# Kernel optimization log

Hardware: AMD Instinct MI355X
Metric: run time of the kernel (lower is better)

Reference implementation:

```python
import jax, jax.numpy as jnp
import numpy as np


def _ln(x, g, b):
    m = x.mean(-1, keepdims=True)
    v = ((x - m) ** 2).mean(-1, keepdims=True)
    return (x - m) * jax.lax.rsqrt(v + 1e-5) * g + b


def _forward(x, fx_in, pre_w1, pre_b1, pre_w2, pre_b2, placeholder,
             ln1_g, ln1_b, px_w, px_b, pfx_w, pfx_b, slice_w, slice_b, temp,
             q_w, k_w, v_w, out_w, out_b, ln2_g, ln2_b,
             mlp_w1, mlp_b1, mlp_w2, mlp_b2,
             ln3_g, ln3_b, head_w1, head_b1, head_w2, head_b2):
    # All linear weights are stored as [in, out] (pre-transposed vs torch nn.Linear).
    B, N, _ = x.shape
    L, H = temp.shape
    dh = slice_w.shape[1]
    gelu = lambda t: jax.nn.gelu(t, approximate=False)
    # preprocess MLP (n_layers=0, res=False): Linear -> GELU -> Linear
    h = jnp.concatenate([x, fx_in], axis=-1)
    h = gelu(h @ pre_w1 + pre_b1) @ pre_w2 + pre_b2
    h = h + placeholder  # learned [D] offset
    scale = 1.0 / jnp.sqrt(jnp.asarray(dh, h.dtype))
    for i in range(L):  # loop over structurally distinct layers
        y = _ln(h, ln1_g[i], ln1_b[i])
        # project to per-head features: bhnd
        fx_mid = (y @ pfx_w[i] + pfx_b[i]).reshape(B, N, H, dh).transpose(0, 2, 1, 3)
        x_mid = (y @ px_w[i] + px_b[i]).reshape(B, N, H, dh).transpose(0, 2, 1, 3)
        # soft slice assignment over G slices
        logits = jnp.einsum('bhnd,dg->bhng', x_mid, slice_w[i]) + slice_b[i]
        sw = jax.nn.softmax(logits / temp[i][None, :, None, None], axis=-1)  # bhng
        norm = sw.sum(axis=2)  # bhg
        tok = jnp.einsum('bhnd,bhng->bhgd', fx_mid, sw) / (norm + 1e-5)[..., None]
        # attention over G=slice_num tokens
        q = tok @ q_w[i]
        k = tok @ k_w[i]
        v = tok @ v_w[i]
        attn = jax.nn.softmax(jnp.einsum('bhgd,bhmd->bhgm', q, k) * scale, axis=-1)
        out_slice = jnp.einsum('bhgm,bhmd->bhgd', attn, v)
        # deslice back to points
        out_x = jnp.einsum('bhgd,bhng->bhnd', out_slice, sw)
        out_x = out_x.transpose(0, 2, 1, 3).reshape(B, N, H * dh)
        h = h + (out_x @ out_w[i] + out_b[i])
        z = _ln(h, ln2_g[i], ln2_b[i])
        h = h + (gelu(z @ mlp_w1[i] + mlp_b1[i]) @ mlp_w2[i] + mlp_b2[i])
    z = _ln(h, ln3_g, ln3_b)
    return gelu(z @ head_w1 + head_b1) @ head_w2 + head_b2


def setup_inputs() -> dict:
    key = jax.random.key(0)
    B, N, D, H, dh, G, L = 2, 16384, 256, 8, 32, 64, 5
    SP, FUN, OUT = 2, 4, 4
    ID = H * dh  # inner_dim == n_hidden
    MR = D * 1   # mlp_ratio=1
    ks = iter(jax.random.split(key, 64))
    nrm = lambda shape, s=0.02: jax.random.normal(next(ks), shape, jnp.float32) * s
    return dict(
        x=jax.random.normal(next(ks), (B, N, SP), jnp.float32),
        fx_in=jax.random.normal(next(ks), (B, N, FUN), jnp.float32),
        pre_w1=nrm((SP + FUN, 2 * D)), pre_b1=jnp.zeros((2 * D,), jnp.float32),
        pre_w2=nrm((2 * D, D)), pre_b2=jnp.zeros((D,), jnp.float32),
        placeholder=nrm((D,)),
        ln1_g=jnp.ones((L, D), jnp.float32), ln1_b=jnp.zeros((L, D), jnp.float32),
        px_w=nrm((L, D, ID)), px_b=jnp.zeros((L, ID), jnp.float32),
        pfx_w=nrm((L, D, ID)), pfx_b=jnp.zeros((L, ID), jnp.float32),
        slice_w=nrm((L, dh, G), 0.1), slice_b=jnp.zeros((L, G), jnp.float32),
        temp=0.5 * jnp.ones((L, H), jnp.float32),
        q_w=nrm((L, dh, dh), 0.1), k_w=nrm((L, dh, dh), 0.1), v_w=nrm((L, dh, dh), 0.1),
        out_w=nrm((L, ID, D)), out_b=jnp.zeros((L, D), jnp.float32),
        ln2_g=jnp.ones((L, D), jnp.float32), ln2_b=jnp.zeros((L, D), jnp.float32),
        mlp_w1=nrm((L, D, MR)), mlp_b1=jnp.zeros((L, MR), jnp.float32),
        mlp_w2=nrm((L, MR, D)), mlp_b2=jnp.zeros((L, D), jnp.float32),
        ln3_g=jnp.ones((D,), jnp.float32), ln3_b=jnp.zeros((D,), jnp.float32),
        head_w1=nrm((D, D)), head_b1=jnp.zeros((D,), jnp.float32),
        head_w2=nrm((D, OUT)), head_b2=jnp.zeros((OUT,), jnp.float32),
    )


def reference(x, fx_in, pre_w1, pre_b1, pre_w2, pre_b2, placeholder,
              ln1_g, ln1_b, px_w, px_b, pfx_w, pfx_b, slice_w, slice_b, temp,
              q_w, k_w, v_w, out_w, out_b, ln2_g, ln2_b,
              mlp_w1, mlp_b1, mlp_w2, mlp_b2,
              ln3_g, ln3_b, head_w1, head_b1, head_w2, head_b2):
    return _forward(x, fx_in, pre_w1, pre_b1, pre_w2, pre_b2, placeholder,
                    ln1_g, ln1_b, px_w, px_b, pfx_w, pfx_b, slice_w, slice_b, temp,
                    q_w, k_w, v_w, out_w, out_b, ln2_g, ln2_b,
                    mlp_w1, mlp_b1, mlp_w2, mlp_b2,
                    ln3_g, ln3_b, head_w1, head_b1, head_w2, head_b2)
```

## Files before the change

kernel.cpp:

```cpp
#include <hip/hip_runtime.h>


#define MTOK 32768
#define NB   16384

typedef unsigned short u16;
using short8 = __attribute__((ext_vector_type(8))) short;
using f4     = __attribute__((ext_vector_type(4))) float;

__device__ __forceinline__ float bfu(u16 u) {
    return __uint_as_float(((unsigned)u) << 16);
}
__device__ __forceinline__ u16 f2bf(float f) {
    unsigned u = __float_as_uint(f);
    u += 0x7FFFu + ((u >> 16) & 1u);
    return (u16)(u >> 16);
}
__device__ __forceinline__ float ldf(const void* p, int i, int isbf) {
    return isbf ? bfu(((const u16*)p)[i]) : ((const float*)p)[i];
}
__device__ __forceinline__ float4 dec4(ushort4 u) {
    return make_float4(bfu(u.x), bfu(u.y), bfu(u.z), bfu(u.w));
}
__device__ __forceinline__ float gelu_f(float x) {
    return 0.5f * x * (1.0f + erff(x * 0.7071067811865475f));
}

typedef __attribute__((address_space(1))) const unsigned int* as1p;
typedef __attribute__((address_space(3))) unsigned int* as3p;
__device__ __forceinline__ void gload_lds16(const u16* g, u16* l) {
    __builtin_amdgcn_global_load_lds((as1p)g, (as3p)l, 16, 0, 0);
}

#define F_H      ((size_t)0)
#define F_OS     ((size_t)8388608)
#define F_TOKP   ((size_t)8421376)
#define F_NORMP  ((size_t)10518528)
#define F_TOK    ((size_t)10584064)
#define F_NORM   ((size_t)10616832)
#define F_BIAS   ((size_t)10617856)
#define F_PARAMS ((size_t)10626048)
#define F_BF     ((size_t)10858884)
#define B_PB2C 0
#define B_OUTB 256
#define B_M1B  1536
#define B_M2B  2816
#define B_HB1  4096
#define B_SP   4352
#define B_END  8192
#define U_WT     ((size_t)0)
#define WT_PRE2  0
#define WT_HEAD1 131072
#define WT_SPFX  196608
#define WT_OUT   1179648
#define WT_MLP1  1507328
#define WT_MLP2  1835008
#define WT_END   2162688
#define U_Y   ((size_t)2162688)
#define U_XM  ((size_t)10551296)
#define U_FM  ((size_t)18939904)
#define U_SW  ((size_t)27328512)

#define P_X    0
#define P_FX   65536
#define P_W1   196608
#define P_B1   199680
#define P_LN1G 200192
#define P_LN1B 201472
#define P_LN2G 202752
#define P_LN2B 204032
#define P_LN3G 205312
#define P_LN3B 205568
#define P_SLW  205824
#define P_SLB  216064
#define P_TEMP 216384
#define P_QW   216448
#define P_KW   221568
#define P_VW   226688
#define P_HW2  231808
#define P_HB2  232832
#define P_END  232836

__global__ __launch_bounds__(256) void cvt_kernel(
    const void* x, const void* fx, const void* w1, const void* b1,
    const void* l1g, const void* l1b, const void* l2g, const void* l2b,
    const void* l3g, const void* l3b, const void* slw, const void* slb,
    const void* tmp, const void* qw, const void* kw, const void* vw,
    const void* hw2, const void* hb2, float* __restrict__ P)
{
    int isbf = (((const u16*)tmp)[0] != 0);
    int idx = blockIdx.x * 256 + threadIdx.x;
    const void* s; int o;
    if      (idx < 65536)  { s = x;   o = idx; }
    else if (idx < 196608) { s = fx;  o = idx - 65536; }
    else if (idx < 199680) { s = w1;  o = idx - 196608; }
    else if (idx < 200192) { s = b1;  o = idx - 199680; }
    else if (idx < 201472) { s = l1g; o = idx - 200192; }
    else if (idx < 202752) { s = l1b; o = idx - 201472; }
    else if (idx < 204032) { s = l2g; o = idx - 202752; }
    else if (idx < 205312) { s = l2b; o = idx - 204032; }
    else if (idx < 205568) { s = l3g; o = idx - 205312; }
    else if (idx < 205824) { s = l3b; o = idx - 205568; }
    else if (idx < 216064) { s = slw; o = idx - 205824; }
    else if (idx < 216384) { s = slb; o = idx - 216064; }
    else if (idx < 216424) { s = tmp; o = idx - 216384; }
    else if (idx < 216448) { return; }
    else if (idx < 221568) { s = qw;  o = idx - 216448; }
    else if (idx < 226688) { s = kw;  o = idx - 221568; }
    else if (idx < 231808) { s = vw;  o = idx - 226688; }
    else if (idx < 232832) { s = hw2; o = idx - 231808; }
    else if (idx < 232836) { s = hb2; o = idx - 232832; }
    else return;
    P[idx] = ldf(s, o, isbf);
}

__global__ __launch_bounds__(256) void prep_main(
    const void* pre_w2, const void* head_w1, const void* pfx_w,
    const void* out_w, const void* mlp_w1, const void* mlp_w2,
    const void* pre_b2, const void* placeholder, const void* pfx_b,
    const void* out_b, const void* mlp_b1, const void* mlp_b2,
    const void* head_b1, const void* tmp,
    u16* __restrict__ WT, float* __restrict__ BIAS)
{
    int isbf = (((const u16*)tmp)[0] != 0);
    int idx = blockIdx.x * 256 + threadIdx.x;
    if (idx < 131072) {
        int n = idx >> 9, k = idx & 511;
        WT[WT_PRE2 + idx] = f2bf(ldf(pre_w2, k * 256 + n, isbf));
    } else if (idx < 196608) {
        int f = idx - 131072;
        int n = f >> 8, k = f & 255;
        WT[WT_HEAD1 + f] = f2bf(ldf(head_w1, k * 256 + n, isbf));
    } else if (idx < 524288) {
        int f = idx - 196608;
        int i = f >> 16, r = f & 65535;
        int n = r >> 8, k = r & 255;
        WT[WT_SPFX + (size_t)i * 196608 + (512 + n) * 256 + k] =
            f2bf(ldf(pfx_w, i * 65536 + k * 256 + n, isbf));
    } else if (idx < 1507328) {
        int f = idx - 524288;
        int mat = f >> 16, r = f & 65535;
        const void* s; int off = (mat % 5) * 65536;
        if      (mat < 5)  s = out_w;
        else if (mat < 10) s = mlp_w1;
        else               s = mlp_w2;
        int n = r >> 8, k = r & 255;
        WT[WT_OUT + f] = f2bf(ldf(s, off + k * 256 + n, isbf));
    } else if (idx < 1507584) {
        int c = idx - 1507328;
        BIAS[B_PB2C + c] = ldf(pre_b2, c, isbf) + ldf(placeholder, c, isbf);
    } else if (idx < 1508864) {
        int o = idx - 1507584; BIAS[B_OUTB + o] = ldf(out_b, o, isbf);
    } else if (idx < 1510144) {
        int o = idx - 1508864; BIAS[B_M1B + o] = ldf(mlp_b1, o, isbf);
    } else if (idx < 1511424) {
        int o = idx - 1510144; BIAS[B_M2B + o] = ldf(mlp_b2, o, isbf);
    } else if (idx < 1511680) {
        int o = idx - 1511424; BIAS[B_HB1 + o] = ldf(head_b1, o, isbf);
    } else if (idx < 1512960) {
        int o = idx - 1511680;
        int i = o >> 8, c = o & 255;
        BIAS[B_SP + i * 768 + 512 + c] = ldf(pfx_b, o, isbf);
    }
}

__global__ __launch_bounds__(256) void prep_pxsl(
    const void* px_w, const void* px_b, const void* slw, const void* slb,
    const void* tmp, u16* __restrict__ WT, float* __restrict__ BIAS)
{
    int isbf = (((const u16*)tmp)[0] != 0);
    __shared__ float pxs[64 * 33];
    __shared__ float sls[2048];
    int blk = blockIdx.x;
    int i = blk >> 5, h = (blk >> 2) & 7, kb = blk & 3;
    int t = threadIdx.x;
#pragma unroll
    for (int p = 0; p < 8; ++p) {
        int flat = t + 256 * p;
        sls[flat] = ldf(slw, i * 2048 + flat, isbf);
        int k = flat >> 5, d = flat & 31;
        pxs[k * 33 + d] = ldf(px_w, i * 65536 + (kb * 64 + k) * 256 + h * 32 + d, isbf);
    }
    __syncthreads();
    int k = t & 63, gb = t >> 6;
    float acc[16];
#pragma unroll
    for (int gi = 0; gi < 16; ++gi) acc[gi] = 0.f;
#pragma unroll
    for (int d = 0; d < 32; ++d) {
        float pv = pxs[k * 33 + d];
        const float* sp = sls + d * 64 + gb * 16;
#pragma unroll
        for (int gi = 0; gi < 16; ++gi) acc[gi] = fmaf(pv, sp[gi], acc[gi]);
    }
    u16* WTp = WT + WT_SPFX + (size_t)i * 196608;
#pragma unroll
    for (int gi = 0; gi < 16; ++gi) {
        int n = h * 64 + gb * 16 + gi;
        WTp[n * 256 + kb * 64 + k] = f2bf(acc[gi]);
    }
    if (kb == 0 && t < 64) {
        int g = t;
        float a = ldf(slb, i * 64 + g, isbf);
#pragma unroll
        for (int d = 0; d < 32; ++d)
            a = fmaf(ldf(px_b, i * 256 + h * 32 + d, isbf), sls[d * 64 + g], a);
        BIAS[B_SP + i * 768 + h * 64 + g] = a;
    }
}

__global__ __launch_bounds__(256) void pre1_kernel(
    const float* __restrict__ P, u16* __restrict__ HID)
{
    __shared__ float w1s[3072];
    __shared__ float b1s[512];
    int t = threadIdx.x;
#pragma unroll
    for (int p = 0; p < 12; ++p) w1s[t + 256 * p] = P[P_W1 + t + 256 * p];
    b1s[t] = P[P_B1 + t];
    b1s[t + 256] = P[P_B1 + t + 256];
    __syncthreads();
    int m = blockIdx.x * 4 + (t >> 6);
    int lane = t & 63;
    float xa = P[P_X + m * 2],      xb = P[P_X + m * 2 + 1];
    float fa = P[P_FX + m * 4],     fb = P[P_FX + m * 4 + 1];
    float fc = P[P_FX + m * 4 + 2], fd = P[P_FX + m * 4 + 3];
    size_t base = (size_t)m * 512 + lane;
#pragma unroll
    for (int jj = 0; jj < 8; ++jj) {
        int j = lane + 64 * jj;
        float a = b1s[j];
        a = fmaf(xa, w1s[j], a);
        a = fmaf(xb, w1s[512 + j], a);
        a = fmaf(fa, w1s[1024 + j], a);
        a = fmaf(fb, w1s[1536 + j], a);
        a = fmaf(fc, w1s[2048 + j], a);
        a = fmaf(fd, w1s[2560 + j], a);
        HID[base + 64 * jj] = f2bf(gelu_f(a));
    }
}

template <int KK, int OMODE>
__global__ __launch_bounds__(256, 4) void gemm_mfma(
    const u16* __restrict__ A, const u16* __restrict__ Wt,
    const float* __restrict__ bias, u16* __restrict__ Cb)
{
    __shared__ u16 As[128 * 64];
    __shared__ u16 Bs[128 * 64];
    const int t = threadIdx.x;
    const int wave = t >> 6, lane = t & 63;
    const int quad = lane >> 4, l15 = lane & 15;
    const int m0 = blockIdx.x * 128;
    const int n0 = blockIdx.y * 128;
    const int wm = (wave & 1) * 64, wn = (wave >> 1) * 64;
    const int r0 = wave * 32;
    const int lrow = lane >> 3, ls = lane & 7;
    f4 acc[4][4];
#pragma unroll
    for (int i = 0; i < 4; ++i)
#pragma unroll
        for (int j = 0; j < 4; ++j) acc[i][j] = (f4){0.f, 0.f, 0.f, 0.f};

    for (int kc = 0; kc < KK; kc += 64) {
        if (kc) __syncthreads();
#pragma unroll
        for (int q = 0; q < 4; ++q) {
            int row = r0 + q * 8 + lrow;
            int chunk = ls ^ (row & 7);
            gload_lds16(A  + (size_t)(m0 + row) * KK + kc + chunk * 8,
                        As + (r0 + q * 8) * 64);
            gload_lds16(Wt + (size_t)(n0 + row) * KK + kc + chunk * 8,
                        Bs + (r0 + q * 8) * 64);
        }
        __syncthreads();
#pragma unroll
        for (int kk = 0; kk < 2; ++kk) {
            short8 a[4], b[4];
#pragma unroll
            for (int i = 0; i < 4; ++i) {
                int R = wm + i * 16 + l15;
                a[i] = *(const short8*)(As + R * 64 + (((quad + kk * 4) ^ (R & 7)) << 3));
            }
#pragma unroll
            for (int j = 0; j < 4; ++j) {
                int R = wn + j * 16 + l15;
                b[j] = *(const short8*)(Bs + R * 64 + (((quad + kk * 4) ^ (R & 7)) << 3));
            }
#pragma unroll
            for (int i = 0; i < 4; ++i)
#pragma unroll
                for (int j = 0; j < 4; ++j)
                    acc[i][j] = __builtin_amdgcn_mfma_f32_16x16x32_bf16(
                        a[i], b[j], acc[i][j], 0, 0, 0);
        }
    }
#pragma unroll
    for (int j = 0; j < 4; ++j) {
        int cj = n0 + wn + j * 16 + l15;
        float bj = bias[cj];
#pragma unroll
        for (int i = 0; i < 4; ++i) {
            int rbase = m0 + wm + i * 16 + quad * 4;
#pragma unroll
            for (int r = 0; r < 4; ++r) {
                float v = acc[i][j][r] + bj;
                size_t off = (size_t)(rbase + r) * 256 + cj;
                if (OMODE == 3) v = gelu_f(v);
                if (OMODE == 1) v += bfu(Cb[off]);
                Cb[off] = f2bf(v);
            }
        }
    }
}

__global__ __launch_bounds__(256, 4) void gemm_spfx(
    const u16* __restrict__ A, const u16* __restrict__ Wt,
    const float* __restrict__ bsp, const float* __restrict__ tempv,
    u16* __restrict__ SW, u16* __restrict__ FM)
{
    __shared__ u16 As[128 * 64];
    __shared__ u16 Bs[128 * 64];
    const int t = threadIdx.x;
    const int wave = t >> 6, lane = t & 63;
    const int quad = lane >> 4, l15 = lane & 15;
    const int m0 = blockIdx.x * 128;
    const int n0 = blockIdx.y * 128;
    const int wm = (wave & 1) * 64, wn = (wave >> 1) * 64;
    const int r0 = wave * 32;
    const int lrow = lane >> 3, ls = lane & 7;
    f4 acc[4][4];
#pragma unroll
    for (int i = 0; i < 4; ++i)
#pragma unroll
        for (int j = 0; j < 4; ++j) acc[i][j] = (f4){0.f, 0.f, 0.f, 0.f};

    for (int kc = 0; kc < 256; kc += 64) {
        if (kc) __syncthreads();
#pragma unroll
        for (int q = 0; q < 4; ++q) {
            int row = r0 + q * 8 + lrow;
            int chunk = ls ^ (row & 7);
            gload_lds16(A  + (size_t)(m0 + row) * 256 + kc + chunk * 8,
                        As + (r0 + q * 8) * 64);
            gload_lds16(Wt + (size_t)(n0 + row) * 256 + kc + chunk * 8,
                        Bs + (r0 + q * 8) * 64);
        }
        __syncthreads();
#pragma unroll
        for (int kk = 0; kk < 2; ++kk) {
            short8 a[4], b[4];
#pragma unroll
            for (int i = 0; i < 4; ++i) {
                int R = wm + i * 16 + l15;
                a[i] = *(const short8*)(As + R * 64 + (((quad + kk * 4) ^ (R & 7)) << 3));
            }
#pragma unroll
            for (int j = 0; j < 4; ++j) {
                int R = wn + j * 16 + l15;
                b[j] = *(const short8*)(Bs + R * 64 + (((quad + kk * 4) ^ (R & 7)) << 3));
            }
#pragma unroll
            for (int i = 0; i < 4; ++i)
#pragma unroll
                for (int j = 0; j < 4; ++j)
                    acc[i][j] = __builtin_amdgcn_mfma_f32_16x16x32_bf16(
                        a[i], b[j], acc[i][j], 0, 0, 0);
        }
    }
    float bj[4];
#pragma unroll
    for (int j = 0; j < 4; ++j) bj[j] = bsp[n0 + wn + j * 16 + l15];
    if (blockIdx.y < 4) {
        const int h = (n0 + wn) >> 6;
        const float itemp = 1.0f / tempv[h];
#pragma unroll
        for (int i = 0; i < 4; ++i) {
#pragma unroll
            for (int r = 0; r < 4; ++r) {
                float v[4];
                float mx = -3.0e38f;
#pragma unroll
                for (int j = 0; j < 4; ++j) {
                    v[j] = (acc[i][j][r] + bj[j]) * itemp;
                    mx = fmaxf(mx, v[j]);
                }
#pragma unroll
                for (int o = 1; o < 16; o <<= 1) mx = fmaxf(mx, __shfl_xor(mx, o));
                float s = 0.f;
#pragma unroll
                for (int j = 0; j < 4; ++j) { v[j] = expf(v[j] - mx); s += v[j]; }
#pragma unroll
                for (int o = 1; o < 16; o <<= 1) s += __shfl_xor(s, o);
                float inv = 1.0f / s;
                int m = m0 + wm + i * 16 + quad * 4 + r;
                int b = m >> 14, n = m & 16383;
                size_t base = (((size_t)(b * 8 + h)) * NB + n) * 64;
#pragma unroll
                for (int j = 0; j < 4; ++j)
                    SW[base + j * 16 + l15] = f2bf(v[j] * inv);
            }
        }
    } else {
        int cj = (n0 - 512) + wn + l15;
#pragma unroll
        for (int j = 0; j < 4; ++j) {
            int col = cj + j * 16;
#pragma unroll
            for (int i = 0; i < 4; ++i) {
                int rbase = m0 + wm + i * 16 + quad * 4;
#pragma unroll
                for (int r = 0; r < 4; ++r)
                    FM[(size_t)(rbase + r) * 256 + col] = f2bf(acc[i][j][r] + bj[j]);
            }
        }
    }
}

__global__ __launch_bounds__(256) void ln_kernel(
    const u16* __restrict__ X, const float* __restrict__ g,
    const float* __restrict__ b, u16* __restrict__ Y)
{
    int lane = threadIdx.x & 63;
    size_t m = (size_t)blockIdx.x * 4 + (threadIdx.x >> 6);
    const float4 x4 = dec4(*(const ushort4*)(X + m * 256 + lane * 4));
    float s = x4.x + x4.y + x4.z + x4.w;
    float q = x4.x * x4.x + x4.y * x4.y + x4.z * x4.z + x4.w * x4.w;
#pragma unroll
    for (int o = 32; o; o >>= 1) { s += __shfl_xor(s, o); q += __shfl_xor(q, o); }
    float mean = s * (1.0f / 256.0f);
    float var = q * (1.0f / 256.0f) - mean * mean;
    float inv = 1.0f / sqrtf(var + 1e-5f);
    const float4 g4 = *(const float4*)(g + lane * 4);
    const float4 b4 = *(const float4*)(b + lane * 4);
    ushort4 y;
    y.x = f2bf((x4.x - mean) * inv * g4.x + b4.x);
    y.y = f2bf((x4.y - mean) * inv * g4.y + b4.y);
    y.z = f2bf((x4.z - mean) * inv * g4.z + b4.z);
    y.w = f2bf((x4.w - mean) * inv * g4.w + b4.w);
    *(ushort4*)(Y + m * 256 + lane * 4) = y;
}

__global__ __launch_bounds__(256) void tok1_kernel(
    const u16* __restrict__ FM, const u16* __restrict__ SW,
    float* __restrict__ TOKP, float* __restrict__ NORMP)
{
    int bh = blockIdx.x >> 6, chunk = blockIdx.x & 63;
    int b = bh >> 3, hd = bh & 7;
    int t = threadIdx.x, wave = t >> 6, lane = t & 63;
    int g0 = (lane >> 3) * 8, d0 = (lane & 7) * 4;
    float4 acc[8];
#pragma unroll
    for (int gi = 0; gi < 8; ++gi) acc[gi] = make_float4(0.f, 0.f, 0.f, 0.f);
    float4 n0a = make_float4(0.f, 0.f, 0.f, 0.f);
    float4 n1a = make_float4(0.f, 0.f, 0.f, 0.f);
    int nbase = chunk * 256 + wave * 64;
    const u16* fmB = FM + ((size_t)b * NB + nbase) * 256 + hd * 32 + d0;
    const u16* swB = SW + ((size_t)bh * NB + nbase) * 64 + g0;
    for (int j = 0; j < 64; ++j) {
        float4 f4v = dec4(*(const ushort4*)(fmB + (size_t)j * 256));
        float4 s0 = dec4(*(const ushort4*)(swB + (size_t)j * 64));
        float4 s1 = dec4(*(const ushort4*)(swB + (size_t)j * 64 + 4));
#define TOKACC(gi, sv)                                            \
        acc[gi].x = fmaf(f4v.x, sv, acc[gi].x);                   \
        acc[gi].y = fmaf(f4v.y, sv, acc[gi].y);                   \
        acc[gi].z = fmaf(f4v.z, sv, acc[gi].z);                   \
        acc[gi].w = fmaf(f4v.w, sv, acc[gi].w);
        TOKACC(0, s0.x) TOKACC(1, s0.y) TOKACC(2, s0.z) TOKACC(3, s0.w)
        TOKACC(4, s1.x) TOKACC(5, s1.y) TOKACC(6, s1.z) TOKACC(7, s1.w)
#undef TOKACC
        n0a.x += s0.x; n0a.y += s0.y; n0a.z += s0.z; n0a.w += s0.w;
        n1a.x += s1.x; n1a.y += s1.y; n1a.z += s1.z; n1a.w += s1.w;
    }
    __shared__ float red[4][2048];
    __shared__ float nred[4][64];
#pragma unroll
    for (int gi = 0; gi < 8; ++gi)
        *(float4*)&red[wave][(g0 + gi) * 32 + d0] = acc[gi];
    if ((lane & 7) == 0) {
        nred[wave][g0 + 0] = n0a.x; nred[wave][g0 + 1] = n0a.y;
        nred[wave][g0 + 2] = n0a.z; nred[wave][g0 + 3] = n0a.w;
        nred[wave][g0 + 4] = n1a.x; nred[wave][g0 + 5] = n1a.y;
        nred[wave][g0 + 6] = n1a.z; nred[wave][g0 + 7] = n1a.w;
    }
    __syncthreads();
    size_t tokBase = (size_t)(chunk * 16 + bh) * 2048;
#pragma unroll
    for (int k = 0; k < 8; ++k) {
        int c = t + 256 * k;
        TOKP[tokBase + c] = red[0][c] + red[1][c] + red[2][c] + red[3][c];
    }
    if (t < 64)
        NORMP[(chunk * 16 + bh) * 64 + t] = nred[0][t] + nred[1][t] + nred[2][t] + nred[3][t];
}

__global__ __launch_bounds__(256) void tok2_kernel(
    const float* __restrict__ TOKP, const float* __restrict__ NORMP,
    float* __restrict__ TOK, float* __restrict__ NORM)
{
    int idx = blockIdx.x * 256 + threadIdx.x;
    if (idx < 32768) {
        int bh = idx >> 11, c = idx & 2047;
        float s = 0.f;
#pragma unroll 8
        for (int ch = 0; ch < 64; ++ch) s += TOKP[(size_t)(ch * 16 + bh) * 2048 + c];
        TOK[idx] = s;
    } else if (idx < 33792) {
        int o = idx - 32768;
        int bh = o >> 6, g = o & 63;
        float s = 0.f;
#pragma unroll 8
        for (int ch = 0; ch < 64; ++ch) s += NORMP[(ch * 16 + bh) * 64 + g];
        NORM[o] = s;
    }
}

__global__ __launch_bounds__(256) void attn_kernel(
    const float* __restrict__ TOK, const float* __restrict__ NORM,
    const float* __restrict__ qw, const float* __restrict__ kw,
    const float* __restrict__ vw, float* __restrict__ OS)
{
    __shared__ float tokd[2048], qs[2048], ks[2048], vs[2048];
    int bh = blockIdx.x;
    int t = threadIdx.x;
#pragma unroll
    for (int i = 0; i < 2; ++i) {
        int f4v = t + 256 * i;
        float4 v = *(const float4*)(TOK + (size_t)bh * 2048 + f4v * 4);
        float inv = 1.0f / (NORM[bh * 64 + (f4v >> 3)] + 1e-5f);
        v.x *= inv; v.y *= inv; v.z *= inv; v.w *= inv;
        *(float4*)&tokd[f4v * 4] = v;
    }
    __syncthreads();
#pragma unroll
    for (int i = 0; i < 8; ++i) {
        int f = t + 256 * i;
        int g = f >> 5, d = f & 31;
        const float* tr = tokd + g * 32;
        float aq = 0.f, ak = 0.f, av = 0.f;
#pragma unroll
        for (int e = 0; e < 32; ++e) {
            float tv = tr[e];
            aq = fmaf(tv, qw[e * 32 + d], aq);
            ak = fmaf(tv, kw[e * 32 + d], ak);
            av = fmaf(tv, vw[e * 32 + d], av);
        }
        qs[f] = aq; ks[f] = ak; vs[f] = av;
    }
    __syncthreads();
    int g = t >> 2, sub = t & 3;
    float4 qv[8];
#pragma unroll
    for (int e4 = 0; e4 < 8; ++e4) qv[e4] = *(const float4*)(qs + g * 32 + e4 * 4);
    float p[16];
    float mx = -3.0e38f;
#pragma unroll
    for (int mm = 0; mm < 16; ++mm) {
        int mI = sub * 16 + mm;
        const float4* kr = (const float4*)(ks + mI * 32);
        float s = 0.f;
#pragma unroll
        for (int e4 = 0; e4 < 8; ++e4) {
            float4 kv = kr[e4];
            s = fmaf(qv[e4].x, kv.x, s); s = fmaf(qv[e4].y, kv.y, s);
            s = fmaf(qv[e4].z, kv.z, s); s = fmaf(qv[e4].w, kv.w, s);
        }
        s *= 0.17677669529663687f;
        p[mm] = s;
        mx = fmaxf(mx, s);
    }
    mx = fmaxf(mx, __shfl_xor(mx, 1));
    mx = fmaxf(mx, __shfl_xor(mx, 2));
    float lsum = 0.f;
#pragma unroll
    for (int mm = 0; mm < 16; ++mm) { p[mm] = expf(p[mm] - mx); lsum += p[mm]; }
    lsum += __shfl_xor(lsum, 1);
    lsum += __shfl_xor(lsum, 2);
    float inv = 1.0f / lsum;
    float4 oa[8];
#pragma unroll
    for (int d4 = 0; d4 < 8; ++d4) oa[d4] = make_float4(0.f, 0.f, 0.f, 0.f);
#pragma unroll
    for (int mm = 0; mm < 16; ++mm) {
        int mI = sub * 16 + mm;
        const float4* vr = (const float4*)(vs + mI * 32);
        float pm = p[mm];
#pragma unroll
        for (int d4 = 0; d4 < 8; ++d4) {
            float4 vv = vr[d4];
            oa[d4].x = fmaf(pm, vv.x, oa[d4].x);
            oa[d4].y = fmaf(pm, vv.y, oa[d4].y);
            oa[d4].z = fmaf(pm, vv.z, oa[d4].z);
            oa[d4].w = fmaf(pm, vv.w, oa[d4].w);
        }
    }
#pragma unroll
    for (int d4 = 0; d4 < 8; ++d4) {
        oa[d4].x += __shfl_xor(oa[d4].x, 1); oa[d4].x += __shfl_xor(oa[d4].x, 2);
        oa[d4].y += __shfl_xor(oa[d4].y, 1); oa[d4].y += __shfl_xor(oa[d4].y, 2);
        oa[d4].z += __shfl_xor(oa[d4].z, 1); oa[d4].z += __shfl_xor(oa[d4].z, 2);
        oa[d4].w += __shfl_xor(oa[d4].w, 1); oa[d4].w += __shfl_xor(oa[d4].w, 2);
    }
    float4 r0 = oa[sub * 2], r1 = oa[sub * 2 + 1];
    r0.x *= inv; r0.y *= inv; r0.z *= inv; r0.w *= inv;
    r1.x *= inv; r1.y *= inv; r1.z *= inv; r1.w *= inv;
    *(float4*)(OS + (size_t)bh * 2048 + g * 32 + sub * 8)     = r0;
    *(float4*)(OS + (size_t)bh * 2048 + g * 32 + sub * 8 + 4) = r1;
}

__global__ __launch_bounds__(256) void deslice_kernel(
    const float* __restrict__ OS, const u16* __restrict__ SW, u16* __restrict__ OX)
{
    __shared__ float swt[8 * 16 * 64];
    int blk = blockIdx.x;
    int b = blk >> 10, n0 = (blk & 1023) * 16;
    int t = threadIdx.x;
    int hd = t >> 5, d = t & 31;
#pragma unroll
    for (int i = 0; i < 8; ++i) {
        int f4v = t + 256 * i;
        int hd2 = f4v >> 8, mm = (f4v >> 4) & 15, g4 = f4v & 15;
        ushort4 u = *(const ushort4*)(SW + (((size_t)(b * 8 + hd2)) * NB + n0 + mm) * 64 + g4 * 4);
        *(float4*)&swt[(hd2 * 16 + mm) * 64 + g4 * 4] = dec4(u);
    }
    __syncthreads();
    float acc[16];
#pragma unroll
    for (int mm = 0; mm < 16; ++mm) acc[mm] = 0.f;
    const float* osb = OS + ((size_t)(b * 8 + hd)) * 2048 + d;
#pragma unroll 4
    for (int g4 = 0; g4 < 16; ++g4) {
        float o0 = osb[(g4 * 4 + 0) * 32], o1 = osb[(g4 * 4 + 1) * 32];
        float o2 = osb[(g4 * 4 + 2) * 32], o3 = osb[(g4 * 4 + 3) * 32];
        const float* swp = swt + hd * 1024 + g4 * 4;
#pragma unroll
        for (int mm = 0; mm < 16; ++mm) {
            float4 sv = *(const float4*)(swp + mm * 64);
            acc[mm] = fmaf(o0, sv.x, fmaf(o1, sv.y, fmaf(o2, sv.z, fmaf(o3, sv.w, acc[mm]))));
        }
    }
#pragma unroll
    for (int mm = 0; mm < 16; ++mm)
        OX[((size_t)b * NB + n0 + mm) * 256 + t] = f2bf(acc[mm]);
}

__global__ __launch_bounds__(256) void head2_kernel(
    const u16* __restrict__ HID, const float* __restrict__ w2,
    const float* __restrict__ b2, const void* tmp, void* __restrict__ OUT)
{
    int isbf = (((const u16*)tmp)[0] != 0);
    int lane = threadIdx.x & 63;
    size_t m = (size_t)blockIdx.x * 4 + (threadIdx.x >> 6);
    const float4 hv = dec4(*(const ushort4*)(HID + m * 256 + lane * 4));
    float4 a = make_float4(0.f, 0.f, 0.f, 0.f);
    float hcomp[4] = {hv.x, hv.y, hv.z, hv.w};
#pragma unroll
    for (int i = 0; i < 4; ++i) {
        const float4 wv = *(const float4*)(w2 + (lane * 4 + i) * 4);
        float h = hcomp[i];
        a.x = fmaf(h, wv.x, a.x); a.y = fmaf(h, wv.y, a.y);
        a.z = fmaf(h, wv.z, a.z); a.w = fmaf(h, wv.w, a.w);
    }
#pragma unroll
    for (int o = 32; o; o >>= 1) {
        a.x += __shfl_xor(a.x, o); a.y += __shfl_xor(a.y, o);
        a.z += __shfl_xor(a.z, o); a.w += __shfl_xor(a.w, o);
    }
    if (lane == 0) {
        float o0 = a.x + b2[0], o1 = a.y + b2[1], o2 = a.z + b2[2], o3 = a.w + b2[3];
        if (isbf) {
            ushort4 r; r.x = f2bf(o0); r.y = f2bf(o1); r.z = f2bf(o2); r.w = f2bf(o3);
            *(ushort4*)((u16*)OUT + m * 4) = r;
        } else {
            *(float4*)((float*)OUT + m * 4) = make_float4(o0, o1, o2, o3);
        }
    }
}

extern "C" void kernel_launch(void* const* d_in, const int* in_sizes, int n_in,
                              void* d_out, int out_size, void* d_ws, size_t ws_size,
                              hipStream_t stream)
{
    const void* x = d_in[0];      const void* fx = d_in[1];
    const void* pre_w1 = d_in[2]; const void* pre_b1 = d_in[3];
    const void* pre_w2 = d_in[4]; const void* pre_b2 = d_in[5];
    const void* placeholder = d_in[6];
    const void* ln1_g = d_in[7];  const void* ln1_b = d_in[8];
    const void* px_w = d_in[9];   const void* px_b = d_in[10];
    const void* pfx_w = d_in[11]; const void* pfx_b = d_in[12];
    const void* slice_w = d_in[13]; const void* slice_b = d_in[14];
    const void* temp = d_in[15];
    const void* q_w = d_in[16];   const void* k_w = d_in[17]; const void* v_w = d_in[18];
    const void* out_w = d_in[19]; const void* out_b = d_in[20];
    const void* ln2_g = d_in[21]; const void* ln2_b = d_in[22];
    const void* mlp_w1 = d_in[23]; const void* mlp_b1 = d_in[24];
    const void* mlp_w2 = d_in[25]; const void* mlp_b2 = d_in[26];
    const void* ln3_g = d_in[27]; const void* ln3_b = d_in[28];
    const void* head_w1 = d_in[29]; const void* head_b1 = d_in[30];
    const void* head_w2 = d_in[31]; const void* head_b2 = d_in[32];

    float* ws = (float*)d_ws;
    u16*   Hb    = (u16*)(ws + F_H);
    float* OSp   = ws + F_OS;
    float* TOKP  = ws + F_TOKP;
    float* NORMP = ws + F_NORMP;
    float* TOKf  = ws + F_TOK;
    float* NORMf = ws + F_NORM;
    float* BIAS  = ws + F_BIAS;
    float* P     = ws + F_PARAMS;
    u16*   U     = (u16*)(ws + F_BF);
    u16*   WT    = U + U_WT;
    u16*   Yb    = U + U_Y;
    u16*   XMb   = U + U_XM;
    u16*   FMb   = U + U_FM;
    u16*   SWb   = U + U_SW;
    u16*   HIDb  = U + U_XM;

    cvt_kernel<<<910, 256, 0, stream>>>(x, fx, pre_w1, pre_b1, ln1_g, ln1_b,
        ln2_g, ln2_b, ln3_g, ln3_b, slice_w, slice_b, temp, q_w, k_w, v_w,
        head_w2, head_b2, P);
    prep_main<<<5910, 256, 0, stream>>>(pre_w2, head_w1, pfx_w, out_w, mlp_w1,
        mlp_w2, pre_b2, placeholder, pfx_b, out_b, mlp_b1, mlp_b2, head_b1,
        temp, WT, BIAS);
    prep_pxsl<<<160, 256, 0, stream>>>(px_w, px_b, slice_w, slice_b, temp, WT, BIAS);
    pre1_kernel<<<8192, 256, 0, stream>>>(P, HIDb);

    dim3 gg(256, 2);
    dim3 gsp(256, 6);
    gemm_mfma<512, 2><<<gg, 256, 0, stream>>>(HIDb, WT + WT_PRE2, BIAS + B_PB2C, Hb);

    for (int i = 0; i < 5; ++i) {
        ln_kernel<<<8192, 256, 0, stream>>>(Hb, P + P_LN1G + i * 256, P + P_LN1B + i * 256, Yb);
        gemm_spfx<<<gsp, 256, 0, stream>>>(Yb, WT + WT_SPFX + (size_t)i * 196608,
            BIAS + B_SP + i * 768, P + P_TEMP + i * 8, SWb, FMb);
        tok1_kernel<<<1024, 256, 0, stream>>>(FMb, SWb, TOKP, NORMP);
        tok2_kernel<<<132, 256, 0, stream>>>(TOKP, NORMP, TOKf, NORMf);
        attn_kernel<<<16, 256, 0, stream>>>(TOKf, NORMf, P + P_QW + i * 1024,
            P + P_KW + i * 1024, P + P_VW + i * 1024, OSp);
        deslice_kernel<<<2048, 256, 0, stream>>>(OSp, SWb, Yb);
        gemm_mfma<256, 1><<<gg, 256, 0, stream>>>(Yb, WT + WT_OUT + i * 65536,
            BIAS + B_OUTB + i * 256, Hb);
        ln_kernel<<<8192, 256, 0, stream>>>(Hb, P + P_LN2G + i * 256, P + P_LN2B + i * 256, Yb);
        gemm_mfma<256, 3><<<gg, 256, 0, stream>>>(Yb, WT + WT_MLP1 + i * 65536,
            BIAS + B_M1B + i * 256, XMb);
        gemm_mfma<256, 1><<<gg, 256, 0, stream>>>(XMb, WT + WT_MLP2 + i * 65536,
            BIAS + B_M2B + i * 256, Hb);
    }

    ln_kernel<<<8192, 256, 0, stream>>>(Hb, P + P_LN3G, P + P_LN3B, Yb);
    gemm_mfma<256, 3><<<gg, 256, 0, stream>>>(Yb, WT + WT_HEAD1, BIAS + B_HB1, XMb);
    head2_kernel<<<8192, 256, 0, stream>>>(XMb, P + P_HW2, P + P_HB2, temp, d_out);
}
```

Measured before the change: 1.134 ms.

## Fuse LayerNorm into residual GEMM epilogues using full-row output tiles

Adds a gemm_ln kernel that computes a 128x256 output tile per block, so each block holds complete rows of the residual stream. Its epilogue adds bias and residual, writes H, reduces row sums through shared memory, and writes the next LayerNorm output. All standalone ln_kernel launches and their extra read/write passes over activations are removed, and the GELU GEMM is specialised. The cost is fewer, larger blocks (256 blocks, launch bounds 2) with more accumulator registers, which lowers occupancy and parallelism in these GEMMs.

```diff
diff --git a/kernel.cpp b/kernel.cpp
--- a/kernel.cpp
+++ b/kernel.cpp
@@ -240,8 +240,114 @@
     }
 }
 
-template <int KK, int OMODE>
-__global__ __launch_bounds__(256, 4) void gemm_mfma(
+template <int KK, bool RES>
+__global__ __launch_bounds__(256, 2) void gemm_ln(
+    const u16* __restrict__ A, const u16* __restrict__ Wt,
+    const float* __restrict__ bias, const float* __restrict__ lng,
+    const float* __restrict__ lnb, u16* __restrict__ Hb, u16* __restrict__ Y)
+{
+    __shared__ u16 As[128 * 64];
+    __shared__ u16 Bs[256 * 64];
+    __shared__ float rs2[2][128], rq2[2][128];
+    const int t = threadIdx.x;
+    const int wave = t >> 6, lane = t & 63;
+    const int quad = lane >> 4, l15 = lane & 15;
+    const int m0 = blockIdx.x * 128;
+    const int wm = (wave & 1) * 64, wn = (wave >> 1) * 128;
+    const int lrow = lane >> 3, ls = lane & 7;
+    f4 acc[4][8];
+#pragma unroll
+    for (int i = 0; i < 4; ++i)
+#pragma unroll
+        for (int j = 0; j < 8; ++j) acc[i][j] = (f4){0.f, 0.f, 0.f, 0.f};
+
+    for (int kc = 0; kc < KK; kc += 64) {
+        if (kc) __syncthreads();
+#pragma unroll
+        for (int q = 0; q < 12; ++q) {
+            int gr = wave * 96 + q * 8;
+            if (gr < 128) {
+                int row = gr + lrow;
+                int chunk = ls ^ (row & 7);
+                gload_lds16(A + (size_t)(m0 + row) * KK + kc + chunk * 8,
+                            As + gr * 64);
+            } else {
+                int brow = gr - 128 + lrow;
+                int chunk = ls ^ (brow & 7);
+                gload_lds16(Wt + (size_t)brow * KK + kc + chunk * 8,
+                            Bs + (gr - 128) * 64);
+            }
+        }
+        __syncthreads();
+#pragma unroll
+        for (int kk = 0; kk < 2; ++kk) {
+            short8 a[4], b[8];
+#pragma unroll
+            for (int i = 0; i < 4; ++i) {
+                int R = wm + i * 16 + l15;
+                a[i] = *(const short8*)(As + R * 64 + (((quad + kk * 4) ^ (R & 7)) << 3));
+            }
+#pragma unroll
+            for (int j = 0; j < 8; ++j) {
+                int Rb = wn + j * 16 + l15;
+                b[j] = *(const short8*)(Bs + Rb * 64 + (((quad + kk * 4) ^ (Rb & 7)) << 3));
+            }
+#pragma unroll
+            for (int i = 0; i < 4; ++i)
+#pragma unroll
+                for (int j = 0; j < 8; ++j)
+                    acc[i][j] = __builtin_amdgcn_mfma_f32_16x16x32_bf16(
+                        a[i], b[j], acc[i][j], 0, 0, 0);
+        }
+    }
+    int colj[8];
+    float bj[8];
+#pragma unroll
+    for (int j = 0; j < 8; ++j) { colj[j] = wn + j * 16 + l15; bj[j] = bias[colj[j]]; }
+    const int half = wn >> 7;
+#pragma unroll
+    for (int i = 0; i < 4; ++i) {
+#pragma unroll
+        for (int r = 0; r < 4; ++r) {
+            int row = wm + i * 16 + quad * 4 + r;
+            size_t gbase = (size_t)(m0 + row) * 256;
+            float s = 0.f, q2 = 0.f;
+#pragma unroll
+            for (int j = 0; j < 8; ++j) {
+                float v = acc[i][j][r] + bj[j];
+                if (RES) v += bfu(Hb[gbase + colj[j]]);
+                Hb[gbase + colj[j]] = f2bf(v);
+                acc[i][j][r] = v;
+                s += v; q2 += v * v;
+            }
+#pragma unroll
+            for (int o = 1; o < 16; o <<= 1) { s += __shfl_xor(s, o); q2 += __shfl_xor(q2, o); }
+            if (l15 == 0) { rs2[half][row] = s; rq2[half][row] = q2; }
+        }
+    }
+    __syncthreads();
+    float gj[8], betj[8];
+#pragma unroll
+    for (int j = 0; j < 8; ++j) { gj[j] = lng[colj[j]]; betj[j] = lnb[colj[j]]; }
+#pragma unroll
+    for (int i = 0; i < 4; ++i) {
+#pragma unroll
+        for (int r = 0; r < 4; ++r) {
+            int row = wm + i * 16 + quad * 4 + r;
+            size_t gbase = (size_t)(m0 + row) * 256;
+            float mean = (rs2[0][row] + rs2[1][row]) * (1.0f / 256.0f);
+            float var = (rq2[0][row] + rq2[1][row]) * (1.0f / 256.0f) - mean * mean;
+            float rstd = rsqrtf(var + 1e-5f);
+#pragma unroll
+            for (int j = 0; j < 8; ++j) {
+                float y = (acc[i][j][r] - mean) * rstd * gj[j] + betj[j];
+                Y[gbase + colj[j]] = f2bf(y);
+            }
+        }
+    }
+}
+
+__global__ __launch_bounds__(256, 4) void gemm_gelu(
     const u16* __restrict__ A, const u16* __restrict__ Wt,
     const float* __restrict__ bias, u16* __restrict__ Cb)
 {
@@ -261,15 +367,15 @@
 #pragma unroll
         for (int j = 0; j < 4; ++j) acc[i][j] = (f4){0.f, 0.f, 0.f, 0.f};
 
-    for (int kc = 0; kc < KK; kc += 64) {
+    for (int kc = 0; kc < 256; kc += 64) {
         if (kc) __syncthreads();
 #pragma unroll
         for (int q = 0; q < 4; ++q) {
             int row = r0 + q * 8 + lrow;
             int chunk = ls ^ (row & 7);
-            gload_lds16(A  + (size_t)(m0 + row) * KK + kc + chunk * 8,
+            gload_lds16(A  + (size_t)(m0 + row) * 256 + kc + chunk * 8,
                         As + (r0 + q * 8) * 64);
-            gload_lds16(Wt + (size_t)(n0 + row) * KK + kc + chunk * 8,
+            gload_lds16(Wt + (size_t)(n0 + row) * 256 + kc + chunk * 8,
                         Bs + (r0 + q * 8) * 64);
         }
         __syncthreads();
@@ -303,11 +409,8 @@
             int rbase = m0 + wm + i * 16 + quad * 4;
 #pragma unroll
             for (int r = 0; r < 4; ++r) {
-                float v = acc[i][j][r] + bj;
-                size_t off = (size_t)(rbase + r) * 256 + cj;
-                if (OMODE == 3) v = gelu_f(v);
-                if (OMODE == 1) v += bfu(Cb[off]);
-                Cb[off] = f2bf(v);
+                float v = gelu_f(acc[i][j][r] + bj);
+                Cb[(size_t)(rbase + r) * 256 + cj] = f2bf(v);
             }
         }
     }
@@ -414,30 +517,6 @@
             }
         }
     }
-}
-
-__global__ __launch_bounds__(256) void ln_kernel(
-    const u16* __restrict__ X, const float* __restrict__ g,
-    const float* __restrict__ b, u16* __restrict__ Y)
-{
-    int lane = threadIdx.x & 63;
-    size_t m = (size_t)blockIdx.x * 4 + (threadIdx.x >> 6);
-    const float4 x4 = dec4(*(const ushort4*)(X + m * 256 + lane * 4));
-    float s = x4.x + x4.y + x4.z + x4.w;
-    float q = x4.x * x4.x + x4.y * x4.y + x4.z * x4.z + x4.w * x4.w;
-#pragma unroll
-    for (int o = 32; o; o >>= 1) { s += __shfl_xor(s, o); q += __shfl_xor(q, o); }
-    float mean = s * (1.0f / 256.0f);
-    float var = q * (1.0f / 256.0f) - mean * mean;
-    float inv = 1.0f / sqrtf(var + 1e-5f);
-    const float4 g4 = *(const float4*)(g + lane * 4);
-    const float4 b4 = *(const float4*)(b + lane * 4);
-    ushort4 y;
-    y.x = f2bf((x4.x - mean) * inv * g4.x + b4.x);
-    y.y = f2bf((x4.y - mean) * inv * g4.y + b4.y);
-    y.z = f2bf((x4.z - mean) * inv * g4.z + b4.z);
-    y.w = f2bf((x4.w - mean) * inv * g4.w + b4.w);
-    *(ushort4*)(Y + m * 256 + lane * 4) = y;
 }
 
 __global__ __launch_bounds__(256) void tok1_kernel(
@@ -724,12 +803,12 @@
     prep_pxsl<<<160, 256, 0, stream>>>(px_w, px_b, slice_w, slice_b, temp, WT, BIAS);
     pre1_kernel<<<8192, 256, 0, stream>>>(P, HIDb);
 
-    dim3 gg(256, 2);
+    dim3 gpl(256, 2);
     dim3 gsp(256, 6);
-    gemm_mfma<512, 2><<<gg, 256, 0, stream>>>(HIDb, WT + WT_PRE2, BIAS + B_PB2C, Hb);
+    gemm_ln<512, false><<<256, 256, 0, stream>>>(HIDb, WT + WT_PRE2,
+        BIAS + B_PB2C, P + P_LN1G, P + P_LN1B, Hb, Yb);
 
     for (int i = 0; i < 5; ++i) {
-        ln_kernel<<<8192, 256, 0, stream>>>(Hb, P + P_LN1G + i * 256, P + P_LN1B + i * 256, Yb);
         gemm_spfx<<<gsp, 256, 0, stream>>>(Yb, WT + WT_SPFX + (size_t)i * 196608,
             BIAS + B_SP + i * 768, P + P_TEMP + i * 8, SWb, FMb);
         tok1_kernel<<<1024, 256, 0, stream>>>(FMb, SWb, TOKP, NORMP);
@@ -737,16 +816,16 @@
         attn_kernel<<<16, 256, 0, stream>>>(TOKf, NORMf, P + P_QW + i * 1024,
             P + P_KW + i * 1024, P + P_VW + i * 1024, OSp);
         deslice_kernel<<<2048, 256, 0, stream>>>(OSp, SWb, Yb);
-        gemm_mfma<256, 1><<<gg, 256, 0, stream>>>(Yb, WT + WT_OUT + i * 65536,
-            BIAS + B_OUTB + i * 256, Hb);
-        ln_kernel<<<8192, 256, 0, stream>>>(Hb, P + P_LN2G + i * 256, P + P_LN2B + i * 256, Yb);
-        gemm_mfma<256, 3><<<gg, 256, 0, stream>>>(Yb, WT + WT_MLP1 + i * 65536,
+        gemm_ln<256, true><<<256, 256, 0, stream>>>(Yb, WT + WT_OUT + i * 65536,
+            BIAS + B_OUTB + i * 256, P + P_LN2G + i * 256, P + P_LN2B + i * 256, Hb, Yb);
+        gemm_gelu<<<gpl, 256, 0, stream>>>(Yb, WT + WT_MLP1 + i * 65536,
             BIAS + B_M1B + i * 256, XMb);
-        gemm_mfma<256, 1><<<gg, 256, 0, stream>>>(XMb, WT + WT_MLP2 + i * 65536,
-            BIAS + B_M2B + i * 256, Hb);
-    }
-
-    ln_kernel<<<8192, 256, 0, stream>>>(Hb, P + P_LN3G, P + P_LN3B, Yb);
-    gemm_mfma<256, 3><<<gg, 256, 0, stream>>>(Yb, WT + WT_HEAD1, BIAS + B_HB1, XMb);
+        const float* ng = (i < 4) ? (P + P_LN1G + (i + 1) * 256) : (P + P_LN3G);
+        const float* nb = (i < 4) ? (P + P_LN1B + (i + 1) * 256) : (P + P_LN3B);
+        gemm_ln<256, true><<<256, 256, 0, stream>>>(XMb, WT + WT_MLP2 + i * 65536,
+            BIAS + B_M2B + i * 256, ng, nb, Hb, Yb);
+    }
+
+    gemm_gelu<<<gpl, 256, 0, stream>>>(Yb, WT + WT_HEAD1, BIAS + B_HB1, XMb);
     head2_kernel<<<8192, 256, 0, stream>>>(XMb, P + P_HW2, P + P_HB2, temp, d_out);
 }
```

New measurement: 1.138 ms. Within noise of the previous version (+0.3%).
